# Performance work log

Hardware: AMD Instinct MI355X
Metric: run time of the kernel (lower is better)

## Reference

```python
import jax, jax.numpy as jnp
import numpy as np

EMBED, IN_DIM, HID, LAYERS, NVIEW = 1024, 256, 256, 3, 6


def _lstm_layer(x_seq, Wih, Whh, bih, bhh):
    # x_seq: [BM, N, D]; torch LSTM gate order i,f,g,o
    BM = x_seq.shape[0]
    h0 = jnp.zeros((BM, HID), x_seq.dtype)
    c0 = jnp.zeros((BM, HID), x_seq.dtype)

    def step(carry, x_t):
        h, c = carry
        gates = x_t @ Wih.T + bih + h @ Whh.T + bhh  # [BM, 4H]
        i, f, g, o = jnp.split(gates, 4, axis=-1)
        c = jax.nn.sigmoid(f) * c + jax.nn.sigmoid(i) * jnp.tanh(g)
        h = jax.nn.sigmoid(o) * jnp.tanh(c)
        return (h, c), h

    _, ys = jax.lax.scan(step, (h0, c0), jnp.swapaxes(x_seq, 0, 1))
    return jnp.swapaxes(ys, 0, 1)  # [BM, N, H]


def setup_inputs() -> dict:
    key = jax.random.key(0)
    ks = jax.random.split(key, 16)
    B, M = 32, 256
    s = lambda fan: 1.0 / np.sqrt(fan)
    inp = {
        "b_x_swin": jax.random.normal(ks[0], (B, M, NVIEW, EMBED), jnp.float32),
        "b_x_conv": jax.random.normal(ks[1], (B, M, NVIEW, EMBED), jnp.float32),
        "Wc": jax.random.uniform(ks[2], (EMBED, EMBED), jnp.float32, -s(EMBED), s(EMBED)),
        "bc": jax.random.uniform(ks[3], (EMBED,), jnp.float32, -s(EMBED), s(EMBED)),
        "Win": jax.random.uniform(ks[4], (IN_DIM, EMBED), jnp.float32, -s(EMBED), s(EMBED)),
        "b_in": jax.random.uniform(ks[5], (IN_DIM,), jnp.float32, -s(EMBED), s(EMBED)),
        "Wih": jax.random.uniform(ks[6], (LAYERS, 4 * HID, IN_DIM), jnp.float32, -s(HID), s(HID)),
        "Whh": jax.random.uniform(ks[7], (LAYERS, 4 * HID, HID), jnp.float32, -s(HID), s(HID)),
        "bih": jax.random.uniform(ks[8], (LAYERS, 4 * HID), jnp.float32, -s(HID), s(HID)),
        "bhh": jax.random.uniform(ks[9], (LAYERS, 4 * HID), jnp.float32, -s(HID), s(HID)),
        "Wv": jax.random.uniform(ks[10], (1, HID), jnp.float32, -s(HID), s(HID)),
        "bv": jax.random.uniform(ks[11], (1,), jnp.float32, -s(HID), s(HID)),
        "Ws": jax.random.uniform(ks[12], (1, NVIEW), jnp.float32, -s(NVIEW), s(NVIEW)),
        "bs": jax.random.uniform(ks[13], (1,), jnp.float32, -s(NVIEW), s(NVIEW)),
    }
    return inp


def reference(b_x_swin, b_x_conv, Wc, bc, Win, b_in, Wih, Whh, bih, bhh, Wv, bv, Ws, bs):
    B, M, N, C = b_x_swin.shape
    # fc_conv + exact GELU + residual (vectorized over all samples; same math as per-sample loop)
    x = b_x_swin + jax.nn.gelu(b_x_conv @ Wc.T + bc, approximate=False)
    x = x @ Win.T + b_in                         # [B, M, N, IN_DIM]
    x = x.reshape(B * M, N, IN_DIM)              # LSTM batch = B*M, seq = N
    for l in range(LAYERS):
        x = _lstm_layer(x, Wih[l], Whh[l], bih[l], bhh[l])
    v = (x @ Wv.T + bv).reshape(B, M, N)         # fc_viewport + flatten(1)
    score = (v @ Ws.T + bs).squeeze(-1)          # fc_score -> [B, M]
    return jnp.mean(score, axis=1)               # torch.mean per sample -> [B]
```

## Files before the change

### kernel.cpp

```cpp
#include <hip/hip_runtime.h>
#include <math.h>

typedef unsigned short u16;
typedef float f32x4 __attribute__((ext_vector_type(4)));
typedef short bf16x8 __attribute__((ext_vector_type(8)));

#define NVIEW 6

__device__ __forceinline__ u16 f2bf(float f){
  unsigned u = __float_as_uint(f);
  u += 0x7FFFu + ((u >> 16) & 1u);
  return (u16)(u >> 16);
}
__device__ __forceinline__ float bf2f(u16 h){
  return __uint_as_float(((unsigned)h) << 16);
}
__device__ __forceinline__ float fsig(float x){
  x = fminf(fmaxf(x, -30.f), 30.f);
  return 1.0f / (1.0f + __expf(-x));
}
__device__ __forceinline__ float ftanh(float x){
  x = fminf(fmaxf(x, -15.f), 15.f);
  float e = __expf(2.0f * x);
  return (e - 1.0f) / (e + 1.0f);
}
__device__ __forceinline__ void gload16(const u16* g, u16* l){
  __builtin_amdgcn_global_load_lds((const __attribute__((address_space(1))) unsigned int*)g,
                                   (__attribute__((address_space(3))) unsigned int*)l,
                                   16, 0, 0);
}

__global__ void k_cvt(const float* __restrict__ in, u16* __restrict__ out, long n4){
  long i = (long)blockIdx.x * blockDim.x + threadIdx.x;
  long stride = (long)gridDim.x * blockDim.x;
  for (; i < n4; i += stride){
    const float4 v = ((const float4*)in)[i];
    ushort4 o;
    o.x = f2bf(v.x); o.y = f2bf(v.y); o.z = f2bf(v.z); o.w = f2bf(v.w);
    ((ushort4*)out)[i] = o;
  }
}

__global__ void k_build_wl(const float* __restrict__ Wih, const float* __restrict__ Whh,
                           u16* __restrict__ Wl){
  int idx = blockIdx.x * 256 + threadIdx.x;
  int l   = idx >> 19;
  int rem = idx & 524287;
  int ro  = rem >> 9;
  int k   = rem & 511;
  int u = ro >> 2, q = ro & 3;
  int ri = q * 256 + u;
  float v = (k < 256) ? Wih[(l * 1024 + ri) * 256 + k]
                      : Whh[(l * 1024 + ri) * 256 + (k - 256)];
  Wl[idx] = f2bf(v);
}

__global__ void k_build_bias(const float* __restrict__ bih, const float* __restrict__ bhh,
                             float* __restrict__ biasL, u16* __restrict__ zbuf){
  int idx = blockIdx.x * 256 + threadIdx.x;
  if (idx < 3072){
    int l = idx >> 10; int ro = idx & 1023;
    int u = ro >> 2, q = ro & 3;
    int ri = q * 256 + u;
    biasL[idx] = bih[l * 1024 + ri] + bhh[l * 1024 + ri];
  }
  if (idx < 256) zbuf[idx] = 0;
}

template<int EPI>
__global__ __launch_bounds__(256)
void gemm_bt(const u16* __restrict__ A0, long sA0,
             const u16* __restrict__ A1, long sA1, int K0,
             const u16* __restrict__ Bm,
             int N, int K,
             const float* __restrict__ bias,
             const float* __restrict__ resid,
             u16* __restrict__ outb,
             float* __restrict__ cbuf,
             int tstep)
{
  __shared__ __align__(16) u16 lA[128 * 64];
  __shared__ __align__(16) u16 lB[128 * 64];

  const int tid  = threadIdx.x;
  const int lane = tid & 63;
  const int wid  = tid >> 6;
  const int wm = wid >> 1, wn = wid & 1;
  const int l15 = lane & 15, lk = lane >> 4;
  const long m0 = (long)blockIdx.x * 128;
  const int  n0 = blockIdx.y * 128;

  f32x4 acc[4][4];
  #pragma unroll
  for (int i = 0; i < 4; ++i)
    #pragma unroll
    for (int j = 0; j < 4; ++j)
      acc[i][j] = (f32x4){0.f, 0.f, 0.f, 0.f};

  const int rowL = tid >> 3;
  const int col8 = (tid & 7) * 8;

  for (int kt = 0; kt < (K >> 6); ++kt){
    const int kbase = kt << 6;
    #pragma unroll
    for (int c = 0; c < 4; ++c){
      int r = c * 32 + rowL;
      int k = kbase + col8;
      const u16* src = (k < K0) ? (A0 + (m0 + r) * sA0 + k)
                                : (A1 + (m0 + r) * sA1 + (k - K0));
      gload16(src, &lA[r * 64 + col8]);
    }
    #pragma unroll
    for (int c = 0; c < 4; ++c){
      int r = c * 32 + rowL;
      int k = kbase + col8;
      gload16(Bm + (long)(n0 + r) * K + k, &lB[r * 64 + col8]);
    }
    __syncthreads();

    #pragma unroll
    for (int ks = 0; ks < 2; ++ks){
      bf16x8 af[4], bfr[4];
      #pragma unroll
      for (int mf = 0; mf < 4; ++mf)
        af[mf] = *(const bf16x8*)&lA[(wm * 64 + mf * 16 + l15) * 64 + ks * 32 + lk * 8];
      #pragma unroll
      for (int nf = 0; nf < 4; ++nf)
        bfr[nf] = *(const bf16x8*)&lB[(wn * 64 + nf * 16 + l15) * 64 + ks * 32 + lk * 8];
      #pragma unroll
      for (int mf = 0; mf < 4; ++mf)
        #pragma unroll
        for (int nf = 0; nf < 4; ++nf)
          acc[mf][nf] = __builtin_amdgcn_mfma_f32_16x16x32_bf16(af[mf], bfr[nf], acc[mf][nf], 0, 0, 0);
    }
    __syncthreads();
  }

  if (EPI == 0 || EPI == 1){
    #pragma unroll
    for (int mf = 0; mf < 4; ++mf){
      #pragma unroll
      for (int nf = 0; nf < 4; ++nf){
        int  n    = n0 + wn * 64 + nf * 16 + l15;
        long mrow = m0 + wm * 64 + mf * 16 + lk * 4;
        float bz = bias[n];
        #pragma unroll
        for (int r = 0; r < 4; ++r){
          float v = acc[mf][nf][r] + bz;
          long off = (mrow + r) * N + n;
          if (EPI == 0){
            float ge = 0.5f * v * (1.0f + erff(v * 0.70710678118654752f));
            v = ge + resid[off];
          }
          outb[off] = f2bf(v);
        }
      }
    }
  } else {
    const int a  = lane & 3;
    const int qb = lane & ~3;
    #pragma unroll
    for (int mf = 0; mf < 4; ++mf){
      #pragma unroll
      for (int nf = 0; nf < 4; ++nf){
        int n = n0 + wn * 64 + nf * 16 + l15;
        float bz = bias[n];
        float v0 = acc[mf][nf][0] + bz;
        float v1 = acc[mf][nf][1] + bz;
        float v2 = acc[mf][nf][2] + bz;
        float v3 = acc[mf][nf][3] + bz;
        float s0 = (a == 0) ? v0 : (a == 1) ? v1 : (a == 2) ? v2 : v3;
        float s1 = (a == 0) ? v1 : (a == 1) ? v2 : (a == 2) ? v3 : v0;
        float s2 = (a == 0) ? v2 : (a == 1) ? v3 : (a == 2) ? v0 : v1;
        float s3 = (a == 0) ? v3 : (a == 1) ? v0 : (a == 2) ? v1 : v2;
        float r0 = s0;
        float r1 = __shfl(s1, qb + ((a + 3) & 3));
        float r2 = __shfl(s2, qb + ((a + 2) & 3));
        float r3 = __shfl(s3, qb + ((a + 1) & 3));
        float wi = (a == 0) ? r0 : (a == 1) ? r1 : (a == 2) ? r2 : r3;
        float wf = (a == 1) ? r0 : (a == 2) ? r1 : (a == 3) ? r2 : r3;
        float wg = (a == 2) ? r0 : (a == 3) ? r1 : (a == 0) ? r2 : r3;
        float wo = (a == 3) ? r0 : (a == 0) ? r1 : (a == 1) ? r2 : r3;
        long row = m0 + wm * 64 + mf * 16 + lk * 4 + a;
        int  u   = ((n0 + wn * 64 + nf * 16) >> 2) + (l15 >> 2);
        float c_old = (tstep == 0) ? 0.0f : cbuf[row * 256 + u];
        float ii = fsig(wi), ff = fsig(wf), gg = ftanh(wg), oo = fsig(wo);
        float cn = ff * c_old + ii * gg;
        float hn = oo * ftanh(cn);
        cbuf[row * 256 + u] = cn;
        outb[(row * NVIEW + tstep) * 256 + u] = f2bf(hn);
      }
    }
  }
}

__global__ void k_score(const u16* __restrict__ X3, const float* __restrict__ Wv,
                        const float* __restrict__ bv, const float* __restrict__ Ws,
                        const float* __restrict__ bs, float* __restrict__ score){
  int lane = threadIdx.x & 63;
  int bm = blockIdx.x * 4 + (threadIdx.x >> 6);
  const u16* row = X3 + (long)bm * (NVIEW * 256);
  float4 wv = *(const float4*)(Wv + lane * 4);
  float p = 0.f;
  #pragma unroll
  for (int n = 0; n < NVIEW; ++n){
    ushort4 xv = *(const ushort4*)(row + n * 256 + lane * 4);
    float d = bf2f(xv.x) * wv.x + bf2f(xv.y) * wv.y + bf2f(xv.z) * wv.z + bf2f(xv.w) * wv.w;
    p += Ws[n] * d;
  }
  #pragma unroll
  for (int off = 32; off; off >>= 1) p += __shfl_xor(p, off);
  if (lane == 0){
    float sw = Ws[0] + Ws[1] + Ws[2] + Ws[3] + Ws[4] + Ws[5];
    score[bm] = p + bv[0] * sw + bs[0];
  }
}

__global__ void k_mean(const float* __restrict__ score, float* __restrict__ out){
  __shared__ float red[256];
  int b = blockIdx.x, tid = threadIdx.x;
  red[tid] = score[b * 256 + tid];
  __syncthreads();
  for (int s = 128; s > 0; s >>= 1){
    if (tid < s) red[tid] += red[tid + s];
    __syncthreads();
  }
  if (tid == 0) out[b] = red[0] * (1.0f / 256.0f);
}

extern "C" void kernel_launch(void* const* d_in, const int* in_sizes, int n_in,
                              void* d_out, int out_size, void* d_ws, size_t ws_size,
                              hipStream_t stream){
  const float* swin = (const float*)d_in[0];
  const float* conv = (const float*)d_in[1];
  const float* Wc   = (const float*)d_in[2];
  const float* bc   = (const float*)d_in[3];
  const float* Win  = (const float*)d_in[4];
  const float* b_in = (const float*)d_in[5];
  const float* Wih  = (const float*)d_in[6];
  const float* Whh  = (const float*)d_in[7];
  const float* bih  = (const float*)d_in[8];
  const float* bhh  = (const float*)d_in[9];
  const float* Wv   = (const float*)d_in[10];
  const float* bv   = (const float*)d_in[11];
  const float* Ws   = (const float*)d_in[12];
  const float* bs   = (const float*)d_in[13];
  float* out = (float*)d_out;

  char* w = (char*)d_ws;
  u16*  convb = (u16*)(w);
  u16*  X0    = (u16*)(w);
  u16*  XA    = (u16*)(w + 25165824);
  u16*  XB    = (u16*)(w + 50331648);
  float* cbuf = (float*)(w + 75497472);
  u16*  Y     = (u16*)(w + 100663296);
  u16*  Wcb   = (u16*)(w + 201326592);
  u16*  Winb  = (u16*)(w + 203423744);
  u16*  Wl    = (u16*)(w + 203948032);
  float* biasL= (float*)(w + 207093760);
  u16*  zbuf  = (u16*)(w + 207106048);
  float* scoreb = (float*)(w + 207106560);

  k_cvt<<<4096, 256, 0, stream>>>(conv, convb, 49152L * 1024 / 4);
  k_cvt<<<512, 256, 0, stream>>>(Wc, Wcb, 1048576 / 4);
  k_cvt<<<128, 256, 0, stream>>>(Win, Winb, 262144 / 4);
  k_build_wl<<<6144, 256, 0, stream>>>(Wih, Whh, Wl);
  k_build_bias<<<12, 256, 0, stream>>>(bih, bhh, biasL, zbuf);

  gemm_bt<0><<<dim3(384, 8), 256, 0, stream>>>(
      convb, 1024L, convb, 1024L, 1024,
      Wcb, 1024, 1024, bc, swin, Y, (float*)nullptr, 0);

  gemm_bt<1><<<dim3(384, 2), 256, 0, stream>>>(
      Y, 1024L, Y, 1024L, 1024,
      Winb, 256, 1024, b_in, (const float*)nullptr, X0, (float*)nullptr, 0);

  const u16* xin = X0;
  u16* xout = XA;
  for (int l = 0; l < 3; ++l){
    for (int t = 0; t < 6; ++t){
      const u16* a1 = (t == 0) ? zbuf : (xout + (t - 1) * 256);
      long s1 = (t == 0) ? 0L : 1536L;
      gemm_bt<2><<<dim3(64, 8), 256, 0, stream>>>(
          xin + t * 256, 1536L, a1, s1, 256,
          Wl + l * 1024 * 512, 1024, 512,
          biasL + l * 1024, (const float*)nullptr,
          xout, cbuf, t);
    }
    if (l == 0){ xin = XA; xout = XB; }
    else if (l == 1){ xin = XB; xout = XA; }
  }

  k_score<<<2048, 256, 0, stream>>>(XA, Wv, bv, Ws, bs, scoreb);
  k_mean<<<32, 256, 0, stream>>>(scoreb, out);
}
```

Baseline: 904.6 us.

## Replace front GEMMs with 256x256-tile 8-wave ping-pong pipelined MFMA kernel

Adds a new GEMM kernel with 256x256 output tiles, 512 threads, double-buffered LDS fed by direct global-to-LDS loads, XOR-swizzled layout, and eight interleaved phases that overlap loads with MFMA under s_setprio. It also swizzles the workgroup order for locality. The two big front GEMMs (fc_conv with GELU plus residual, and the input projection) now use it instead of the 128x128 gemm_bt. The larger tile raises data reuse and the pipelining hides memory latency. The cost is higher register and LDS pressure, and the input-projection launch has only 192 workgroups.

```diff
diff --git a/kernel.cpp b/kernel.cpp
--- a/kernel.cpp
+++ b/kernel.cpp
@@ -65,6 +65,141 @@
     biasL[idx] = bih[l * 1024 + ri] + bhh[l * 1024 + ri];
   }
   if (idx < 256) zbuf[idx] = 0;
+}
+
+template<int EPI>
+__global__ __launch_bounds__(512, 2)
+void gemm8p(const u16* __restrict__ A, long sA,
+            const u16* __restrict__ Bm, long sB,
+            int N, int K,
+            const float* __restrict__ bias,
+            const float* __restrict__ resid,
+            u16* __restrict__ outb)
+{
+  __shared__ __align__(16) u16 shA[2 * 16384];
+  __shared__ __align__(16) u16 shB[2 * 16384];
+
+  const int tid  = threadIdx.x;
+  const int lane = tid & 63;
+  const int wv   = tid >> 6;
+  const int wm   = wv >> 2;
+  const int wn   = wv & 3;
+  const int wm16 = wm * 16, wn16 = wn * 16;
+  const int l15  = lane & 15, lk = lane >> 4;
+  const int w2   = wv * 2;
+
+  const int nwg = gridDim.x;
+  const int qq  = nwg >> 3;
+  const int b   = blockIdx.x;
+  const int swz = (b & 7) * qq + (b >> 3);
+  const int NB  = N >> 8;
+  const long m0 = (long)(swz / NB) * 256;
+  const int  n0 = (swz % NB) * 256;
+
+  const int NT = K >> 6;
+
+  const long laneA = (long)(lane >> 3) * sA + (long)(((lane & 7) ^ (lane >> 3)) << 3);
+  const long laneB = (long)(lane >> 3) * sB + (long)(((lane & 7) ^ (lane >> 3)) << 3);
+
+  auto STA = [&](int buf, int mh, int t){
+    if (t < NT){
+      #pragma unroll
+      for (int j = 0; j < 2; ++j){
+        const int chunk = w2 + j;
+        gload16(A + (m0 + mh * 128 + chunk * 8) * sA + (long)t * 64 + laneA,
+                shA + buf * 16384 + mh * 8192 + chunk * 512 + lane * 8);
+      }
+    }
+  };
+  auto STB = [&](int buf, int nh, int t){
+    if (t < NT){
+      #pragma unroll
+      for (int j = 0; j < 2; ++j){
+        const int chunk = w2 + j;
+        gload16(Bm + (long)(n0 + nh * 128 + chunk * 8) * sB + (long)t * 64 + laneB,
+                shB + buf * 16384 + nh * 8192 + chunk * 512 + lane * 8);
+      }
+    }
+  };
+
+  f32x4 acc[8][4];
+  #pragma unroll
+  for (int i = 0; i < 8; ++i)
+    #pragma unroll
+    for (int j = 0; j < 4; ++j)
+      acc[i][j] = (f32x4){0.f, 0.f, 0.f, 0.f};
+
+  STA(0, 0, 0); STB(0, 0, 0); STA(0, 1, 0); STB(0, 1, 0);
+  STA(1, 0, 1); STB(1, 1, 1);
+  asm volatile("s_waitcnt vmcnt(4)" ::: "memory");
+  asm volatile("s_barrier" ::: "memory");
+
+#define PH(BUF, MH, NH, STG, VM)                                              \
+  {                                                                           \
+    bf16x8 af[2][4], bq[2][2];                                                \
+    _Pragma("unroll") for (int ks = 0; ks < 2; ++ks){                         \
+      _Pragma("unroll") for (int i = 0; i < 4; ++i){                          \
+        const int row  = ((MH) * 4 + i) * 32 + wm16 + l15;                    \
+        const int slot = (ks * 4 + lk) ^ (l15 & 7);                           \
+        af[ks][i] = *(const bf16x8*)&shA[(BUF) * 16384 + row * 64 + slot * 8];\
+      }                                                                       \
+      _Pragma("unroll") for (int j = 0; j < 2; ++j){                          \
+        const int rn   = ((NH) * 2 + j) * 64 + wn16 + l15;                    \
+        const int slot = (ks * 4 + lk) ^ (l15 & 7);                           \
+        bq[ks][j] = *(const bf16x8*)&shB[(BUF) * 16384 + rn * 64 + slot * 8]; \
+      }                                                                       \
+    }                                                                         \
+    STG;                                                                      \
+    asm volatile("s_barrier" ::: "memory");                                   \
+    asm volatile("s_waitcnt lgkmcnt(0)" ::: "memory");                        \
+    __builtin_amdgcn_s_setprio(1);                                            \
+    _Pragma("unroll") for (int i = 0; i < 4; ++i)                             \
+      _Pragma("unroll") for (int j = 0; j < 2; ++j)                           \
+        _Pragma("unroll") for (int ks = 0; ks < 2; ++ks)                      \
+          acc[(MH)*4 + i][(NH)*2 + j] = __builtin_amdgcn_mfma_f32_16x16x32_bf16( \
+              af[ks][i], bq[ks][j], acc[(MH)*4 + i][(NH)*2 + j], 0, 0, 0);    \
+    __builtin_amdgcn_s_setprio(0);                                            \
+    VM;                                                                       \
+    asm volatile("s_barrier" ::: "memory");                                   \
+  }
+
+  const int NIT = NT >> 1;
+  for (int it = 0; it < NIT; ++it){
+    const int t1 = 2 * it + 1;
+    const bool lastit = (it == NIT - 1);
+    PH(0, 0, 0, STB(1, 0, t1), ;);
+    PH(0, 1, 0, STA(1, 1, t1), ;);
+    PH(0, 0, 1, STB(0, 0, t1 + 1), ;);
+    PH(0, 1, 1, STA(0, 0, t1 + 1),
+       if (lastit) { asm volatile("s_waitcnt vmcnt(0)" ::: "memory"); }
+       else        { asm volatile("s_waitcnt vmcnt(4)" ::: "memory"); });
+    PH(1, 0, 0, STA(0, 1, t1 + 1), ;);
+    PH(1, 0, 1, STB(0, 1, t1 + 1), ;);
+    PH(1, 1, 1, STA(1, 0, t1 + 2), ;);
+    PH(1, 1, 0, STB(1, 1, t1 + 2),
+       asm volatile("s_waitcnt vmcnt(4)" ::: "memory"););
+  }
+#undef PH
+
+  #pragma unroll
+  for (int mf = 0; mf < 8; ++mf){
+    #pragma unroll
+    for (int nf = 0; nf < 4; ++nf){
+      const int n = n0 + nf * 64 + wn16 + l15;
+      const float bz = bias[n];
+      const long mrow = m0 + mf * 32 + wm16 + lk * 4;
+      #pragma unroll
+      for (int r = 0; r < 4; ++r){
+        float v = acc[mf][nf][r] + bz;
+        const long off = (mrow + r) * (long)N + n;
+        if (EPI == 0){
+          float ge = 0.5f * v * (1.0f + erff(v * 0.70710678118654752f));
+          v = ge + resid[off];
+        }
+        outb[off] = f2bf(v);
+      }
+    }
+  }
 }
 
 template<int EPI>
@@ -267,13 +402,11 @@
   k_build_wl<<<6144, 256, 0, stream>>>(Wih, Whh, Wl);
   k_build_bias<<<12, 256, 0, stream>>>(bih, bhh, biasL, zbuf);
 
-  gemm_bt<0><<<dim3(384, 8), 256, 0, stream>>>(
-      convb, 1024L, convb, 1024L, 1024,
-      Wcb, 1024, 1024, bc, swin, Y, (float*)nullptr, 0);
-
-  gemm_bt<1><<<dim3(384, 2), 256, 0, stream>>>(
-      Y, 1024L, Y, 1024L, 1024,
-      Winb, 256, 1024, b_in, (const float*)nullptr, X0, (float*)nullptr, 0);
+  gemm8p<0><<<768, 512, 0, stream>>>(convb, 1024L, Wcb, 1024L,
+                                     1024, 1024, bc, swin, Y);
+
+  gemm8p<1><<<192, 512, 0, stream>>>(Y, 1024L, Winb, 1024L,
+                                     256, 1024, b_in, (const float*)nullptr, X0);
 
   const u16* xin = X0;
   u16* xout = XA;
```

Result: faster. 861.3 us (-4.8%).

## Pipeline GEMM K-loop with 5-slot swizzled LDS ring and cheaper GELU

Applied to the files above, without the earlier changes.

Replaces the single-buffered 64-wide K loop with a 32-wide K tile held in a 5-slot LDS ring. Four stages are prefetched ahead, and explicit vmcnt waits plus raw barriers overlap global-to-LDS loads with MFMA compute. An XOR swizzle on LDS columns reduces bank conflicts. Exact erff in the GELU epilogue is swapped for an Abramowitz-Stegun polynomial with __expf, and launch bounds request 2 blocks per CU. LDS use rises to 80KB per block, which may limit occupancy. The erf approximation adds a small error.

```diff
diff --git a/kernel.cpp b/kernel.cpp
--- a/kernel.cpp
+++ b/kernel.cpp
@@ -1,5 +1,6 @@
 #include <hip/hip_runtime.h>
 #include <math.h>
+#include <stdint.h>
 
 typedef unsigned short u16;
 typedef float f32x4 __attribute__((ext_vector_type(4)));
@@ -23,6 +24,15 @@
   x = fminf(fmaxf(x, -15.f), 15.f);
   float e = __expf(2.0f * x);
   return (e - 1.0f) / (e + 1.0f);
+}
+__device__ __forceinline__ float gelu_exact(float v){
+  float x  = v * 0.70710678118654752f;
+  float ax = fabsf(x);
+  float t  = 1.0f / fmaf(0.3275911f, ax, 1.0f);
+  float p  = t * fmaf(t, fmaf(t, fmaf(t, fmaf(t, 1.061405429f, -1.453152027f),
+                                      1.421413741f), -0.284496736f), 0.254829592f);
+  float er = copysignf(1.0f - p * __expf(-ax * ax), x);
+  return 0.5f * v * (1.0f + er);
 }
 __device__ __forceinline__ void gload16(const u16* g, u16* l){
   __builtin_amdgcn_global_load_lds((const __attribute__((address_space(1))) unsigned int*)g,
@@ -68,10 +78,10 @@
 }
 
 template<int EPI>
-__global__ __launch_bounds__(256)
-void gemm_bt(const u16* __restrict__ A0, long sA0,
+__global__ __launch_bounds__(256, 2)
+void gemm_dr(const u16* __restrict__ A0, long sA0,
              const u16* __restrict__ A1, long sA1, int K0,
-             const u16* __restrict__ Bm,
+             const u16* __restrict__ Bm, long sB,
              int N, int K,
              const float* __restrict__ bias,
              const float* __restrict__ resid,
@@ -79,8 +89,8 @@
              float* __restrict__ cbuf,
              int tstep)
 {
-  __shared__ __align__(16) u16 lA[128 * 64];
-  __shared__ __align__(16) u16 lB[128 * 64];
+  __shared__ __align__(16) u16 lA[5 * 4096];
+  __shared__ __align__(16) u16 lB[5 * 4096];
 
   const int tid  = threadIdx.x;
   const int lane = tid & 63;
@@ -89,6 +99,30 @@
   const int l15 = lane & 15, lk = lane >> 4;
   const long m0 = (long)blockIdx.x * 128;
   const int  n0 = blockIdx.y * 128;
+  const int  NT = K >> 5;
+
+  const int rA0  = tid >> 2;
+  const int cA   = tid & 3;
+  const int scol = (cA ^ (rA0 & 3)) << 3;
+  const int ldst = rA0 * 32 + cA * 8;
+
+  auto STAGE = [&](int slot, int t){
+    const int kb = t << 5;
+    const int so = slot * 4096;
+    #pragma unroll
+    for (int c = 0; c < 2; ++c){
+      const int r  = c * 64 + rA0;
+      const int gc = kb + scol;
+      const u16* s = (gc < K0) ? (A0 + (m0 + r) * sA0 + gc)
+                               : (A1 + (m0 + r) * sA1 + (gc - K0));
+      gload16(s, &lA[so + c * 2048 + ldst]);
+    }
+    #pragma unroll
+    for (int c = 0; c < 2; ++c){
+      const int r = c * 64 + rA0;
+      gload16(Bm + (long)(n0 + r) * sB + (kb + scol), &lB[so + c * 2048 + ldst]);
+    }
+  };
 
   f32x4 acc[4][4];
   #pragma unroll
@@ -97,44 +131,45 @@
     for (int j = 0; j < 4; ++j)
       acc[i][j] = (f32x4){0.f, 0.f, 0.f, 0.f};
 
-  const int rowL = tid >> 3;
-  const int col8 = (tid & 7) * 8;
-
-  for (int kt = 0; kt < (K >> 6); ++kt){
-    const int kbase = kt << 6;
-    #pragma unroll
-    for (int c = 0; c < 4; ++c){
-      int r = c * 32 + rowL;
-      int k = kbase + col8;
-      const u16* src = (k < K0) ? (A0 + (m0 + r) * sA0 + k)
-                                : (A1 + (m0 + r) * sA1 + (k - K0));
-      gload16(src, &lA[r * 64 + col8]);
-    }
-    #pragma unroll
-    for (int c = 0; c < 4; ++c){
-      int r = c * 32 + rowL;
-      int k = kbase + col8;
-      gload16(Bm + (long)(n0 + r) * K + k, &lB[r * 64 + col8]);
-    }
-    __syncthreads();
-
-    #pragma unroll
-    for (int ks = 0; ks < 2; ++ks){
-      bf16x8 af[4], bfr[4];
-      #pragma unroll
-      for (int mf = 0; mf < 4; ++mf)
-        af[mf] = *(const bf16x8*)&lA[(wm * 64 + mf * 16 + l15) * 64 + ks * 32 + lk * 8];
+  const int rdA = (wm * 64 + l15) * 32 + ((lk ^ (l15 & 3)) << 3);
+  const int rdB = (wn * 64 + l15) * 32 + ((lk ^ (l15 & 3)) << 3);
+
+  auto COMPUTE = [&](int slot){
+    const int so = slot * 4096;
+    bf16x8 af[4], bq[4];
+    #pragma unroll
+    for (int mf = 0; mf < 4; ++mf)
+      af[mf] = *(const bf16x8*)&lA[so + rdA + mf * 512];
+    #pragma unroll
+    for (int nf = 0; nf < 4; ++nf)
+      bq[nf] = *(const bf16x8*)&lB[so + rdB + nf * 512];
+    #pragma unroll
+    for (int mf = 0; mf < 4; ++mf)
       #pragma unroll
       for (int nf = 0; nf < 4; ++nf)
-        bfr[nf] = *(const bf16x8*)&lB[(wn * 64 + nf * 16 + l15) * 64 + ks * 32 + lk * 8];
-      #pragma unroll
-      for (int mf = 0; mf < 4; ++mf)
-        #pragma unroll
-        for (int nf = 0; nf < 4; ++nf)
-          acc[mf][nf] = __builtin_amdgcn_mfma_f32_16x16x32_bf16(af[mf], bfr[nf], acc[mf][nf], 0, 0, 0);
-    }
-    __syncthreads();
-  }
+        acc[mf][nf] = __builtin_amdgcn_mfma_f32_16x16x32_bf16(af[mf], bq[nf], acc[mf][nf], 0, 0, 0);
+  };
+
+  STAGE(0, 0); STAGE(1, 1); STAGE(2, 2); STAGE(3, 3);
+
+  int sr = 0, sw = 4;
+  for (int t = 0; t + 4 <= NT; ++t){
+    asm volatile("s_waitcnt vmcnt(12)" ::: "memory");
+    asm volatile("s_barrier" ::: "memory");
+    if (t + 4 < NT){ STAGE(sw, t + 4); }
+    COMPUTE(sr);
+    sr = (sr == 4) ? 0 : sr + 1;
+    sw = (sw == 4) ? 0 : sw + 1;
+  }
+  asm volatile("s_waitcnt vmcnt(8)" ::: "memory");
+  asm volatile("s_barrier" ::: "memory");
+  COMPUTE(sr); sr = (sr == 4) ? 0 : sr + 1;
+  asm volatile("s_waitcnt vmcnt(4)" ::: "memory");
+  asm volatile("s_barrier" ::: "memory");
+  COMPUTE(sr); sr = (sr == 4) ? 0 : sr + 1;
+  asm volatile("s_waitcnt vmcnt(0)" ::: "memory");
+  asm volatile("s_barrier" ::: "memory");
+  COMPUTE(sr);
 
   if (EPI == 0 || EPI == 1){
     #pragma unroll
@@ -148,10 +183,7 @@
         for (int r = 0; r < 4; ++r){
           float v = acc[mf][nf][r] + bz;
           long off = (mrow + r) * N + n;
-          if (EPI == 0){
-            float ge = 0.5f * v * (1.0f + erff(v * 0.70710678118654752f));
-            v = ge + resid[off];
-          }
+          if (EPI == 0) v = gelu_exact(v) + resid[off];
           outb[off] = f2bf(v);
         }
       }
@@ -267,13 +299,13 @@
   k_build_wl<<<6144, 256, 0, stream>>>(Wih, Whh, Wl);
   k_build_bias<<<12, 256, 0, stream>>>(bih, bhh, biasL, zbuf);
 
-  gemm_bt<0><<<dim3(384, 8), 256, 0, stream>>>(
+  gemm_dr<0><<<dim3(384, 8), 256, 0, stream>>>(
       convb, 1024L, convb, 1024L, 1024,
-      Wcb, 1024, 1024, bc, swin, Y, (float*)nullptr, 0);
-
-  gemm_bt<1><<<dim3(384, 2), 256, 0, stream>>>(
+      Wcb, 1024L, 1024, 1024, bc, swin, Y, (float*)nullptr, 0);
+
+  gemm_dr<1><<<dim3(384, 2), 256, 0, stream>>>(
       Y, 1024L, Y, 1024L, 1024,
-      Winb, 256, 1024, b_in, (const float*)nullptr, X0, (float*)nullptr, 0);
+      Winb, 1024L, 256, 1024, b_in, (const float*)nullptr, X0, (float*)nullptr, 0);
 
   const u16* xin = X0;
   u16* xout = XA;
@@ -281,9 +313,9 @@
     for (int t = 0; t < 6; ++t){
       const u16* a1 = (t == 0) ? zbuf : (xout + (t - 1) * 256);
       long s1 = (t == 0) ? 0L : 1536L;
-      gemm_bt<2><<<dim3(64, 8), 256, 0, stream>>>(
+      gemm_dr<2><<<dim3(64, 8), 256, 0, stream>>>(
           xin + t * 256, 1536L, a1, s1, 256,
-          Wl + l * 1024 * 512, 1024, 512,
+          Wl + l * 1024 * 512, 512L, 1024, 512,
           biasL + l * 1024, (const float*)nullptr,
           xout, cbuf, t);
     }
```

After: 756.1 us. 16.4% less time.
